# Optimization experiments

Hardware: AMD Instinct MI355X
Metric: run time of the kernel (lower is better)

## Reference

```python
import jax, jax.numpy as jnp
import numpy as np

NUM_CAPSULE = 32
DIM_CAPSULE = 16
ROUTINGS = 3
IN_CAPS = 144
IN_DIM = 8
EPS = 1e-7  # keras.backend.epsilon()


def setup_inputs() -> dict:
    key = jax.random.key(0)
    k1, k2 = jax.random.split(key)
    inputs = jax.random.normal(k1, (512, IN_CAPS, IN_DIM), dtype=jnp.float32)
    # glorot_uniform over shape [num_capsule, 144, dim_capsule, 8]
    fan_in, fan_out = IN_CAPS * IN_DIM, NUM_CAPSULE * DIM_CAPSULE
    limit = np.sqrt(6.0 / (fan_in + fan_out)).astype(np.float32)
    W = jax.random.uniform(k2, (NUM_CAPSULE, IN_CAPS, DIM_CAPSULE, IN_DIM),
                           minval=-limit, maxval=limit, dtype=jnp.float32)
    return {"inputs": inputs, "W": W}


def _squash(s):
    # s: [..., dim_capsule]
    n2 = jnp.sum(s * s, axis=-1, keepdims=True)
    return (n2 / (1.0 + n2)) * s / jnp.sqrt(n2 + EPS)


def reference(inputs, W):
    # inputs: [B, 144, 8]; W: [num_capsule, 144, dim_capsule, 8]
    # tile+einsum('abci,bcji->abcj') == broadcasted contraction over i
    inputs_hat = jnp.einsum('aci,bcji->abcj', inputs, W)  # [B, nc, 144, dc]
    b = jnp.zeros(inputs_hat.shape[:3], dtype=inputs_hat.dtype)  # [B, nc, 144]
    outputs = None
    for i in range(ROUTINGS):
        c = jax.nn.softmax(b, axis=1)                      # over num_capsule
        s = jnp.einsum('abc,abcd->abd', c, inputs_hat)     # [B, nc, dc]
        outputs = _squash(s)
        if i < ROUTINGS - 1:
            b = b + jnp.einsum('abd,abcd->abc', outputs, inputs_hat)
    return outputs
```

## Files before the change

### kernel.cpp

```cpp
#include <hip/hip_runtime.h>

#define NC 32
#define DC 16
#define INC 144
#define IND 8
#define NT 512

#define HBS 1168
#define HH_OFF (NC * HBS + 8)
#define LGW_OFF (HH_OFF + NC * HBS)
#define LG_S 152
#define OH_OFF (LGW_OFF + NC * LG_S)
#define SMEM_HALVES (OH_OFF + NC * DC)
#define SMEM_BYTES (SMEM_HALVES * 2)

typedef _Float16 h2 __attribute__((ext_vector_type(2)));
typedef _Float16 h4 __attribute__((ext_vector_type(4)));
typedef _Float16 h8 __attribute__((ext_vector_type(8)));
typedef float f4 __attribute__((ext_vector_type(4)));

union H8 { h8 v; h2 p[4]; };

#if __has_builtin(__builtin_amdgcn_fdot2)
__device__ __forceinline__ float fdot2(h2 a, h2 b, float c) {
    return __builtin_amdgcn_fdot2(a, b, c, false);
}
#else
__device__ __forceinline__ float fdot2(h2 a, h2 b, float c) {
    return c + (float)a[0] * (float)b[0] + (float)a[1] * (float)b[1];
}
#endif

__global__ void convw_kernel(const float* __restrict__ W, _Float16* __restrict__ Wh) {
    int i = blockIdx.x * 256 + threadIdx.x;
    f4 v = reinterpret_cast<const f4*>(W)[i];
    h4 h;
    h[0] = (_Float16)v[0]; h[1] = (_Float16)v[1];
    h[2] = (_Float16)v[2]; h[3] = (_Float16)v[3];
    reinterpret_cast<h4*>(Wh)[i] = h;
}

__device__ __forceinline__ float squash16(float s) {
    float n2 = s * s;
    n2 += __shfl_xor(n2, 1, 16);
    n2 += __shfl_xor(n2, 2, 16);
    n2 += __shfl_xor(n2, 4, 16);
    n2 += __shfl_xor(n2, 8, 16);
    return s * (n2 / ((1.0f + n2) * sqrtf(n2 + 1e-7f)));
}

template <typename WT>
__global__ __launch_bounds__(NT)
void caps_kernel(const float* __restrict__ xg, const WT* __restrict__ Wg,
                 float* __restrict__ out) {
    extern __shared__ _Float16 sm[];
    _Float16* lg = sm + LGW_OFF;
    _Float16* o_h = sm + OH_OFF;
    _Float16* x_h = lg;

    const int t = threadIdx.x;
    const int b = t >> 4;
    const int d = t & 15;
    const int a = blockIdx.x;

    if (t < (INC * IND) / 4) {
        f4 v = reinterpret_cast<const f4*>(xg + (size_t)a * (INC * IND))[t];
        h4 h;
        h[0] = (_Float16)v[0]; h[1] = (_Float16)v[1];
        h[2] = (_Float16)v[2]; h[3] = (_Float16)v[3];
        *reinterpret_cast<h4*>(x_h + t * 4) = h;
    }
    __syncthreads();

    _Float16* hw = sm + (d < 8 ? (b * HBS + d) : (HH_OFF + b * HBS + (d - 8)));

    float s0 = 0.0f;
    {
        const WT* wp = Wg + ((size_t)(b * INC) * DC + d) * IND;
        #pragma unroll 8
        for (int c = 0; c < INC; ++c) {
            H8 xv;
            xv.v = *reinterpret_cast<const h8*>(x_h + c * IND);
            float acc;
            if constexpr (sizeof(WT) == 2) {
                H8 wv;
                wv.v = *reinterpret_cast<const h8*>(wp + (size_t)c * (DC * IND));
                acc = fdot2(wv.p[0], xv.p[0], 0.f);
                acc = fdot2(wv.p[1], xv.p[1], acc);
                acc = fdot2(wv.p[2], xv.p[2], acc);
                acc = fdot2(wv.p[3], xv.p[3], acc);
            } else {
                const float* wf = reinterpret_cast<const float*>(wp) + (size_t)c * (DC * IND);
                f4 w0 = *reinterpret_cast<const f4*>(wf);
                f4 w1 = *reinterpret_cast<const f4*>(wf + 4);
                acc = (float)xv.v[0] * w0[0];
                acc = fmaf((float)xv.v[1], w0[1], acc);
                acc = fmaf((float)xv.v[2], w0[2], acc);
                acc = fmaf((float)xv.v[3], w0[3], acc);
                acc = fmaf((float)xv.v[4], w1[0], acc);
                acc = fmaf((float)xv.v[5], w1[1], acc);
                acc = fmaf((float)xv.v[6], w1[2], acc);
                acc = fmaf((float)xv.v[7], w1[3], acc);
            }
            s0 += acc;
            hw[c * 8] = (_Float16)acc;
            (void)0;
        }
    }
    {
        float o0 = squash16(s0 * (1.0f / 32.0f));
        o_h[t] = (_Float16)o0;
    }
    __syncthreads();

    float lgr[9] = {0.f, 0.f, 0.f, 0.f, 0.f, 0.f, 0.f, 0.f, 0.f};

    for (int it = 0; it < 2; ++it) {
        {
            H8 oL, oH;
            oL.v = *reinterpret_cast<const h8*>(o_h + b * DC);
            oH.v = *reinterpret_cast<const h8*>(o_h + b * DC + 8);
            #pragma unroll
            for (int k = 0; k < 9; ++k) {
                const int c = d + DC * k;
                H8 hl, hh;
                hl.v = *reinterpret_cast<const h8*>(sm + b * HBS + c * 8);
                hh.v = *reinterpret_cast<const h8*>(sm + HH_OFF + b * HBS + c * 8);
                float dot = fdot2(hl.p[0], oL.p[0], 0.f);
                dot = fdot2(hl.p[1], oL.p[1], dot);
                dot = fdot2(hl.p[2], oL.p[2], dot);
                dot = fdot2(hl.p[3], oL.p[3], dot);
                dot = fdot2(hh.p[0], oH.p[0], dot);
                dot = fdot2(hh.p[1], oH.p[1], dot);
                dot = fdot2(hh.p[2], oH.p[2], dot);
                dot = fdot2(hh.p[3], oH.p[3], dot);
                lgr[k] += dot;
                lg[b * LG_S + c] = (_Float16)lgr[k];
            }
        }
        __syncthreads();

        if (t < INC) {
            const int c = t;
            float m = -1e30f;
            for (int bb = 0; bb < NC; ++bb)
                m = fmaxf(m, (float)lg[bb * LG_S + c]);
            float S = 0.f;
            for (int bb = 0; bb < NC; ++bb) {
                float e = __expf((float)lg[bb * LG_S + c] - m);
                S += e;
                lg[bb * LG_S + c] = (_Float16)e;
            }
            float inv = 1.0f / S;
            for (int bb = 0; bb < NC; ++bb)
                lg[bb * LG_S + c] = (_Float16)((float)lg[bb * LG_S + c] * inv);
        }
        __syncthreads();

        {
            const _Float16* cp = lg + b * LG_S;
            float s = 0.f;
            #pragma unroll 8
            for (int c = 0; c < INC; ++c)
                s = fmaf((float)cp[c], (float)hw[c * 8], s);
            float oo = squash16(s);
            if (it == 0) {
                o_h[t] = (_Float16)oo;
            } else {
                out[(size_t)a * (NC * DC) + t] = oo;
            }
        }
        if (it == 0) __syncthreads();
    }
}

extern "C" void kernel_launch(void* const* d_in, const int* in_sizes, int n_in,
                              void* d_out, int out_size, void* d_ws, size_t ws_size,
                              hipStream_t stream) {
    const float* x = (const float*)d_in[0];
    const float* W = (const float*)d_in[1];
    float* out = (float*)d_out;

    const size_t WH_BYTES = (size_t)NC * INC * DC * IND * 2;

    if (ws_size >= WH_BYTES) {
        _Float16* Wh = (_Float16*)d_ws;
        hipLaunchKernelGGL(convw_kernel, dim3((NC * INC * DC * IND / 4) / 256),
                           dim3(256), 0, stream, W, Wh);
        hipFuncSetAttribute(reinterpret_cast<const void*>(&caps_kernel<_Float16>),
                            hipFuncAttributeMaxDynamicSharedMemorySize, SMEM_BYTES);
        hipLaunchKernelGGL(caps_kernel<_Float16>, dim3(512), dim3(NT), SMEM_BYTES,
                           stream, x, Wh, out);
    } else {
        hipFuncSetAttribute(reinterpret_cast<const void*>(&caps_kernel<float>),
                            hipFuncAttributeMaxDynamicSharedMemorySize, SMEM_BYTES);
        hipLaunchKernelGGL(caps_kernel<float>, dim3(512), dim3(NT), SMEM_BYTES,
                           stream, x, W, out);
    }
}
```

Measured before the change: 53.54 us.

## Split capsule routing across 1024 threads with transposed logits and parallel softmax

Doubles the block to 1024 threads, splitting the 144 input capsules into two halves whose partial sums are combined through shared memory. The logits are stored transposed (input-capsule-major) so the softmax reads contiguous rows, and two threads share each softmax with vector loads and a shuffle reduction. The intent is to cut the per-thread serial work and the slow strided softmax. The cost is extra barriers and partial-sum exchanges, and the larger block may cut occupancy or raise register pressure under the new launch bound.

```diff
diff --git a/kernel.cpp b/kernel.cpp
--- a/kernel.cpp
+++ b/kernel.cpp
@@ -4,14 +4,15 @@
 #define DC 16
 #define INC 144
 #define IND 8
-#define NT 512
+#define NT 1024
 
 #define HBS 1168
 #define HH_OFF (NC * HBS + 8)
-#define LGW_OFF (HH_OFF + NC * HBS)
-#define LG_S 152
-#define OH_OFF (LGW_OFF + NC * LG_S)
-#define SMEM_HALVES (OH_OFF + NC * DC)
+#define LGT_OFF (HH_OFF + NC * HBS)
+#define LGT_S 36
+#define OH_OFF (LGT_OFF + INC * LGT_S)
+#define PS_OFF (OH_OFF + NC * DC)
+#define SMEM_HALVES (PS_OFF + 512 * 2)
 #define SMEM_BYTES (SMEM_HALVES * 2)
 
 typedef _Float16 h2 __attribute__((ext_vector_type(2)));
@@ -50,25 +51,29 @@
 }
 
 template <typename WT>
-__global__ __launch_bounds__(NT)
+__global__ __launch_bounds__(NT, 4)
 void caps_kernel(const float* __restrict__ xg, const WT* __restrict__ Wg,
                  float* __restrict__ out) {
     extern __shared__ _Float16 sm[];
-    _Float16* lg = sm + LGW_OFF;
+    _Float16* lg = sm + LGT_OFF;
     _Float16* o_h = sm + OH_OFF;
+    float* ps = reinterpret_cast<float*>(sm + PS_OFF);
     _Float16* x_h = lg;
 
     const int t = threadIdx.x;
-    const int b = t >> 4;
-    const int d = t & 15;
+    const int h = t >> 9;
+    const int u = t & 511;
+    const int b = u >> 4;
+    const int d = u & 15;
     const int a = blockIdx.x;
+    const int c0 = h * 72;
 
     if (t < (INC * IND) / 4) {
         f4 v = reinterpret_cast<const f4*>(xg + (size_t)a * (INC * IND))[t];
-        h4 h;
-        h[0] = (_Float16)v[0]; h[1] = (_Float16)v[1];
-        h[2] = (_Float16)v[2]; h[3] = (_Float16)v[3];
-        *reinterpret_cast<h4*>(x_h + t * 4) = h;
+        h4 hv;
+        hv[0] = (_Float16)v[0]; hv[1] = (_Float16)v[1];
+        hv[2] = (_Float16)v[2]; hv[3] = (_Float16)v[3];
+        *reinterpret_cast<h4*>(x_h + t * 4) = hv;
     }
     __syncthreads();
 
@@ -76,21 +81,21 @@
 
     float s0 = 0.0f;
     {
-        const WT* wp = Wg + ((size_t)(b * INC) * DC + d) * IND;
+        const WT* wp = Wg + ((size_t)(b * INC + c0) * DC + d) * IND;
         #pragma unroll 8
-        for (int c = 0; c < INC; ++c) {
+        for (int c = c0; c < c0 + 72; ++c) {
             H8 xv;
             xv.v = *reinterpret_cast<const h8*>(x_h + c * IND);
             float acc;
             if constexpr (sizeof(WT) == 2) {
                 H8 wv;
-                wv.v = *reinterpret_cast<const h8*>(wp + (size_t)c * (DC * IND));
+                wv.v = *reinterpret_cast<const h8*>(wp);
                 acc = fdot2(wv.p[0], xv.p[0], 0.f);
                 acc = fdot2(wv.p[1], xv.p[1], acc);
                 acc = fdot2(wv.p[2], xv.p[2], acc);
                 acc = fdot2(wv.p[3], xv.p[3], acc);
             } else {
-                const float* wf = reinterpret_cast<const float*>(wp) + (size_t)c * (DC * IND);
+                const float* wf = reinterpret_cast<const float*>(wp);
                 f4 w0 = *reinterpret_cast<const f4*>(wf);
                 f4 w1 = *reinterpret_cast<const f4*>(wf + 4);
                 acc = (float)xv.v[0] * w0[0];
@@ -102,18 +107,21 @@
                 acc = fmaf((float)xv.v[6], w1[2], acc);
                 acc = fmaf((float)xv.v[7], w1[3], acc);
             }
+            wp += DC * IND;
             s0 += acc;
             hw[c * 8] = (_Float16)acc;
-            (void)0;
-        }
-    }
-    {
-        float o0 = squash16(s0 * (1.0f / 32.0f));
-        o_h[t] = (_Float16)o0;
-    }
+        }
+    }
+    if (h) ps[u] = s0;
     __syncthreads();
-
-    float lgr[9] = {0.f, 0.f, 0.f, 0.f, 0.f, 0.f, 0.f, 0.f, 0.f};
+    if (!h) {
+        float s0t = s0 + ps[u];
+        o_h[u] = (_Float16)squash16(s0t * (1.0f / 32.0f));
+    }
+    __syncthreads();
+
+    const int NK = h ? 4 : 5;
+    float lgr[5] = {0.f, 0.f, 0.f, 0.f, 0.f};
 
     for (int it = 0; it < 2; ++it) {
         {
@@ -121,56 +129,75 @@
             oL.v = *reinterpret_cast<const h8*>(o_h + b * DC);
             oH.v = *reinterpret_cast<const h8*>(o_h + b * DC + 8);
             #pragma unroll
-            for (int k = 0; k < 9; ++k) {
-                const int c = d + DC * k;
-                H8 hl, hh;
-                hl.v = *reinterpret_cast<const h8*>(sm + b * HBS + c * 8);
-                hh.v = *reinterpret_cast<const h8*>(sm + HH_OFF + b * HBS + c * 8);
-                float dot = fdot2(hl.p[0], oL.p[0], 0.f);
-                dot = fdot2(hl.p[1], oL.p[1], dot);
-                dot = fdot2(hl.p[2], oL.p[2], dot);
-                dot = fdot2(hl.p[3], oL.p[3], dot);
-                dot = fdot2(hh.p[0], oH.p[0], dot);
-                dot = fdot2(hh.p[1], oH.p[1], dot);
-                dot = fdot2(hh.p[2], oH.p[2], dot);
-                dot = fdot2(hh.p[3], oH.p[3], dot);
-                lgr[k] += dot;
-                lg[b * LG_S + c] = (_Float16)lgr[k];
+            for (int q = 0; q < 5; ++q) {
+                if (q < NK) {
+                    const int c = d + DC * (h + 2 * q);
+                    H8 hl, hu;
+                    hl.v = *reinterpret_cast<const h8*>(sm + b * HBS + c * 8);
+                    hu.v = *reinterpret_cast<const h8*>(sm + HH_OFF + b * HBS + c * 8);
+                    float dot = fdot2(hl.p[0], oL.p[0], 0.f);
+                    dot = fdot2(hl.p[1], oL.p[1], dot);
+                    dot = fdot2(hl.p[2], oL.p[2], dot);
+                    dot = fdot2(hl.p[3], oL.p[3], dot);
+                    dot = fdot2(hu.p[0], oH.p[0], dot);
+                    dot = fdot2(hu.p[1], oH.p[1], dot);
+                    dot = fdot2(hu.p[2], oH.p[2], dot);
+                    dot = fdot2(hu.p[3], oH.p[3], dot);
+                    lgr[q] += dot;
+                    lg[c * LGT_S + b] = (_Float16)lgr[q];
+                }
             }
         }
         __syncthreads();
 
-        if (t < INC) {
-            const int c = t;
-            float m = -1e30f;
-            for (int bb = 0; bb < NC; ++bb)
-                m = fmaxf(m, (float)lg[bb * LG_S + c]);
+        if (t < 2 * INC) {
+            const int c = t >> 1;
+            const int hh = t & 1;
+            _Float16* row = lg + c * LGT_S + hh * 16;
+            float v[16];
+            #pragma unroll
+            for (int j = 0; j < 4; ++j) {
+                h4 r = *reinterpret_cast<const h4*>(row + 4 * j);
+                v[4 * j + 0] = (float)r[0]; v[4 * j + 1] = (float)r[1];
+                v[4 * j + 2] = (float)r[2]; v[4 * j + 3] = (float)r[3];
+            }
+            float m = v[0];
+            #pragma unroll
+            for (int j = 1; j < 16; ++j) m = fmaxf(m, v[j]);
+            m = fmaxf(m, __shfl_xor(m, 1));
             float S = 0.f;
-            for (int bb = 0; bb < NC; ++bb) {
-                float e = __expf((float)lg[bb * LG_S + c] - m);
-                S += e;
-                lg[bb * LG_S + c] = (_Float16)e;
-            }
+            #pragma unroll
+            for (int j = 0; j < 16; ++j) { v[j] = __expf(v[j] - m); S += v[j]; }
+            S += __shfl_xor(S, 1);
             float inv = 1.0f / S;
-            for (int bb = 0; bb < NC; ++bb)
-                lg[bb * LG_S + c] = (_Float16)((float)lg[bb * LG_S + c] * inv);
+            #pragma unroll
+            for (int j = 0; j < 4; ++j) {
+                h4 r;
+                r[0] = (_Float16)(v[4 * j + 0] * inv);
+                r[1] = (_Float16)(v[4 * j + 1] * inv);
+                r[2] = (_Float16)(v[4 * j + 2] * inv);
+                r[3] = (_Float16)(v[4 * j + 3] * inv);
+                *reinterpret_cast<h4*>(row + 4 * j) = r;
+            }
         }
         __syncthreads();
 
         {
-            const _Float16* cp = lg + b * LG_S;
+            const _Float16* cp0 = lg + b;
             float s = 0.f;
             #pragma unroll 8
-            for (int c = 0; c < INC; ++c)
-                s = fmaf((float)cp[c], (float)hw[c * 8], s);
-            float oo = squash16(s);
-            if (it == 0) {
-                o_h[t] = (_Float16)oo;
-            } else {
-                out[(size_t)a * (NC * DC) + t] = oo;
-            }
-        }
-        if (it == 0) __syncthreads();
+            for (int c = c0; c < c0 + 72; ++c)
+                s = fmaf((float)cp0[c * LGT_S], (float)hw[c * 8], s);
+            if (h) ps[u] = s;
+            __syncthreads();
+            if (!h) {
+                float st = s + ps[u];
+                float oo = squash16(st);
+                if (it == 0) o_h[u] = (_Float16)oo;
+                else out[(size_t)a * (NC * DC) + u] = oo;
+            }
+            if (it == 0) __syncthreads();
+        }
     }
 }
 
```

Result: no change. 52.82 us (-1.3%).

## Keep inputs_hat in registers and compute agreement via packed-half shuffle reductions

Applied to the files above, without the earlier changes.

Each thread now holds its 144 fp16 inputs_hat values in registers (72 packed halves) instead of writing them to a large shared-memory buffer. The agreement dot products use a butterfly reduce-scatter with shuffles inside each 16-lane group, and the softmax is split across two threads per input capsule using register arrays. Shared memory drops to a small static allocation, which removes the dynamic-smem attribute call and may let more blocks fit per CU. The cost is heavy register pressure from 72 h2 registers plus full unrolling, which could cap occupancy or cause spills, and more of the reduction now runs in fp16.

```diff
diff --git a/kernel.cpp b/kernel.cpp
--- a/kernel.cpp
+++ b/kernel.cpp
@@ -1,18 +1,12 @@
 #include <hip/hip_runtime.h>
+#include <utility>
 
 #define NC 32
 #define DC 16
 #define INC 144
 #define IND 8
 #define NT 512
-
-#define HBS 1168
-#define HH_OFF (NC * HBS + 8)
-#define LGW_OFF (HH_OFF + NC * HBS)
 #define LG_S 152
-#define OH_OFF (LGW_OFF + NC * LG_S)
-#define SMEM_HALVES (OH_OFF + NC * DC)
-#define SMEM_BYTES (SMEM_HALVES * 2)
 
 typedef _Float16 h2 __attribute__((ext_vector_type(2)));
 typedef _Float16 h4 __attribute__((ext_vector_type(4)));
@@ -20,6 +14,16 @@
 typedef float f4 __attribute__((ext_vector_type(4)));
 
 union H8 { h8 v; h2 p[4]; };
+union HU { h2 h; unsigned u; };
+
+template <class F, int... Is>
+__device__ __forceinline__ void sfor_impl(F&& f, std::integer_sequence<int, Is...>) {
+    (f(std::integral_constant<int, Is>{}), ...);
+}
+template <int N, class F>
+__device__ __forceinline__ void sfor(F&& f) {
+    sfor_impl((F&&)f, std::make_integer_sequence<int, N>{});
+}
 
 #if __has_builtin(__builtin_amdgcn_fdot2)
 __device__ __forceinline__ float fdot2(h2 a, h2 b, float c) {
@@ -53,10 +57,8 @@
 __global__ __launch_bounds__(NT)
 void caps_kernel(const float* __restrict__ xg, const WT* __restrict__ Wg,
                  float* __restrict__ out) {
-    extern __shared__ _Float16 sm[];
-    _Float16* lg = sm + LGW_OFF;
-    _Float16* o_h = sm + OH_OFF;
-    _Float16* x_h = lg;
+    __shared__ _Float16 x_h[INC * IND];
+    __shared__ _Float16 lg[NC * LG_S];
 
     const int t = threadIdx.x;
     const int b = t >> 4;
@@ -65,20 +67,19 @@
 
     if (t < (INC * IND) / 4) {
         f4 v = reinterpret_cast<const f4*>(xg + (size_t)a * (INC * IND))[t];
-        h4 h;
-        h[0] = (_Float16)v[0]; h[1] = (_Float16)v[1];
-        h[2] = (_Float16)v[2]; h[3] = (_Float16)v[3];
-        *reinterpret_cast<h4*>(x_h + t * 4) = h;
+        h4 hv;
+        hv[0] = (_Float16)v[0]; hv[1] = (_Float16)v[1];
+        hv[2] = (_Float16)v[2]; hv[3] = (_Float16)v[3];
+        *reinterpret_cast<h4*>(x_h + t * 4) = hv;
     }
     __syncthreads();
 
-    _Float16* hw = sm + (d < 8 ? (b * HBS + d) : (HH_OFF + b * HBS + (d - 8)));
-
+    h2 hreg[72];
     float s0 = 0.0f;
     {
         const WT* wp = Wg + ((size_t)(b * INC) * DC + d) * IND;
-        #pragma unroll 8
-        for (int c = 0; c < INC; ++c) {
+        sfor<INC>([&](auto C) {
+            constexpr int c = C.value;
             H8 xv;
             xv.v = *reinterpret_cast<const h8*>(x_h + c * IND);
             float acc;
@@ -103,74 +104,113 @@
                 acc = fmaf((float)xv.v[7], w1[3], acc);
             }
             s0 += acc;
-            hw[c * 8] = (_Float16)acc;
-            (void)0;
-        }
-    }
-    {
-        float o0 = squash16(s0 * (1.0f / 32.0f));
-        o_h[t] = (_Float16)o0;
-    }
-    __syncthreads();
-
-    float lgr[9] = {0.f, 0.f, 0.f, 0.f, 0.f, 0.f, 0.f, 0.f, 0.f};
+            hreg[c >> 1][c & 1] = (_Float16)acc;
+        });
+    }
+    float o = squash16(s0 * (1.0f / 32.0f));
+
+    float lgr[9];
+    sfor<9>([&](auto J) { lgr[J.value] = 0.f; });
 
     for (int it = 0; it < 2; ++it) {
         {
-            H8 oL, oH;
-            oL.v = *reinterpret_cast<const h8*>(o_h + b * DC);
-            oH.v = *reinterpret_cast<const h8*>(o_h + b * DC + 8);
-            #pragma unroll
-            for (int k = 0; k < 9; ++k) {
-                const int c = d + DC * k;
-                H8 hl, hh;
-                hl.v = *reinterpret_cast<const h8*>(sm + b * HBS + c * 8);
-                hh.v = *reinterpret_cast<const h8*>(sm + HH_OFF + b * HBS + c * 8);
-                float dot = fdot2(hl.p[0], oL.p[0], 0.f);
-                dot = fdot2(hl.p[1], oL.p[1], dot);
-                dot = fdot2(hl.p[2], oL.p[2], dot);
-                dot = fdot2(hl.p[3], oL.p[3], dot);
-                dot = fdot2(hh.p[0], oH.p[0], dot);
-                dot = fdot2(hh.p[1], oH.p[1], dot);
-                dot = fdot2(hh.p[2], oH.p[2], dot);
-                dot = fdot2(hh.p[3], oH.p[3], dot);
-                lgr[k] += dot;
-                lg[b * LG_S + c] = (_Float16)lgr[k];
-            }
+            h2 oh2;
+            oh2[0] = (_Float16)o; oh2[1] = (_Float16)o;
+            sfor<9>([&](auto J) {
+                constexpr int j = J.value;
+                h2 qp[8];
+                sfor<8>([&](auto I) {
+                    constexpr int i = I.value;
+                    qp[i] = oh2 * hreg[8 * j + i];
+                });
+                const bool h8s = (d & 8) != 0;
+                sfor<4>([&](auto I) {
+                    constexpr int i = I.value;
+                    h2 send = h8s ? qp[i] : qp[i + 4];
+                    h2 keep = h8s ? qp[i + 4] : qp[i];
+                    HU su; su.h = send;
+                    HU ru; ru.u = __shfl_xor(su.u, 8, 16);
+                    qp[i] = keep + ru.h;
+                });
+                const bool h4s = (d & 4) != 0;
+                sfor<2>([&](auto I) {
+                    constexpr int i = I.value;
+                    h2 send = h4s ? qp[i] : qp[i + 2];
+                    h2 keep = h4s ? qp[i + 2] : qp[i];
+                    HU su; su.h = send;
+                    HU ru; ru.u = __shfl_xor(su.u, 4, 16);
+                    qp[i] = keep + ru.h;
+                });
+                {
+                    const bool h2s = (d & 2) != 0;
+                    h2 send = h2s ? qp[0] : qp[1];
+                    h2 keep = h2s ? qp[1] : qp[0];
+                    HU su; su.h = send;
+                    HU ru; ru.u = __shfl_xor(su.u, 2, 16);
+                    qp[0] = keep + ru.h;
+                }
+                {
+                    HU su; su.h = qp[0];
+                    HU ru; ru.u = __shfl_xor(su.u, 1, 16);
+                    h2 tot = qp[0] + ru.h;
+                    HU tu; tu.h = tot;
+                    unsigned short sel = (d & 1) ? (unsigned short)(tu.u >> 16)
+                                                 : (unsigned short)(tu.u & 0xffffu);
+                    union { unsigned short s; _Float16 hv; } cv;
+                    cv.s = sel;
+                    lgr[j] += (float)cv.hv;
+                }
+                lg[b * LG_S + 16 * j + d] = (_Float16)lgr[j];
+            });
         }
         __syncthreads();
 
-        if (t < INC) {
-            const int c = t;
-            float m = -1e30f;
-            for (int bb = 0; bb < NC; ++bb)
-                m = fmaxf(m, (float)lg[bb * LG_S + c]);
+        if (t < 2 * INC) {
+            const int c = t >> 1;
+            const int hh = t & 1;
+            float v[16];
+            sfor<16>([&](auto I) {
+                constexpr int i = I.value;
+                v[i] = (float)lg[(hh * 16 + i) * LG_S + c];
+            });
+            float m = v[0];
+            sfor<15>([&](auto I) { m = fmaxf(m, v[I.value + 1]); });
+            m = fmaxf(m, __shfl_xor(m, 1));
             float S = 0.f;
-            for (int bb = 0; bb < NC; ++bb) {
-                float e = __expf((float)lg[bb * LG_S + c] - m);
-                S += e;
-                lg[bb * LG_S + c] = (_Float16)e;
-            }
+            sfor<16>([&](auto I) {
+                constexpr int i = I.value;
+                v[i] = __expf(v[i] - m);
+                S += v[i];
+            });
+            S += __shfl_xor(S, 1);
             float inv = 1.0f / S;
-            for (int bb = 0; bb < NC; ++bb)
-                lg[bb * LG_S + c] = (_Float16)((float)lg[bb * LG_S + c] * inv);
+            sfor<16>([&](auto I) {
+                constexpr int i = I.value;
+                lg[(hh * 16 + i) * LG_S + c] = (_Float16)(v[i] * inv);
+            });
         }
         __syncthreads();
 
         {
             const _Float16* cp = lg + b * LG_S;
-            float s = 0.f;
-            #pragma unroll 8
-            for (int c = 0; c < INC; ++c)
-                s = fmaf((float)cp[c], (float)hw[c * 8], s);
-            float oo = squash16(s);
+            float sA = 0.f, sB = 0.f;
+            sfor<18>([&](auto M) {
+                constexpr int m2 = M.value;
+                H8 cc;
+                cc.v = *reinterpret_cast<const h8*>(cp + m2 * 8);
+                sA = fdot2(cc.p[0], hreg[m2 * 4 + 0], sA);
+                sB = fdot2(cc.p[1], hreg[m2 * 4 + 1], sB);
+                sA = fdot2(cc.p[2], hreg[m2 * 4 + 2], sA);
+                sB = fdot2(cc.p[3], hreg[m2 * 4 + 3], sB);
+            });
+            float oo = squash16(sA + sB);
             if (it == 0) {
-                o_h[t] = (_Float16)oo;
+                o = oo;
+                __syncthreads();
             } else {
                 out[(size_t)a * (NC * DC) + t] = oo;
             }
         }
-        if (it == 0) __syncthreads();
     }
 }
 
@@ -187,14 +227,10 @@
         _Float16* Wh = (_Float16*)d_ws;
         hipLaunchKernelGGL(convw_kernel, dim3((NC * INC * DC * IND / 4) / 256),
                            dim3(256), 0, stream, W, Wh);
-        hipFuncSetAttribute(reinterpret_cast<const void*>(&caps_kernel<_Float16>),
-                            hipFuncAttributeMaxDynamicSharedMemorySize, SMEM_BYTES);
-        hipLaunchKernelGGL(caps_kernel<_Float16>, dim3(512), dim3(NT), SMEM_BYTES,
+        hipLaunchKernelGGL(caps_kernel<_Float16>, dim3(512), dim3(NT), 0,
                            stream, x, Wh, out);
     } else {
-        hipFuncSetAttribute(reinterpret_cast<const void*>(&caps_kernel<float>),
-                            hipFuncAttributeMaxDynamicSharedMemorySize, SMEM_BYTES);
-        hipLaunchKernelGGL(caps_kernel<float>, dim3(512), dim3(NT), SMEM_BYTES,
+        hipLaunchKernelGGL(caps_kernel<float>, dim3(512), dim3(NT), 0,
                            stream, x, W, out);
     }
 }
```

Result: slower. 70.01 us (+30.8%).

## Keep inputs_hat in registers and reorder W for coalesced per-thread capsule loads

Applied to the files above, without the earlier changes.

Each thread now owns 9 input capsules for one output capsule and holds all 16 inputs_hat dimensions in registers, instead of spilling the full inputs_hat tensor into ~150KB of shared memory. The W conversion kernel reorders W into a layout that matches this thread mapping so fp16 loads coalesce. Softmax is split across two threads per input capsule with shuffles, and the squash reduction runs through cross-lane butterflies. This removes the large LDS footprint to allow more blocks per CU, at the cost of heavy register use (18 h8 vectors plus 16 accumulators) and many shuffles.

```diff
diff --git a/kernel.cpp b/kernel.cpp
--- a/kernel.cpp
+++ b/kernel.cpp
@@ -5,21 +5,14 @@
 #define INC 144
 #define IND 8
 #define NT 512
-
-#define HBS 1168
-#define HH_OFF (NC * HBS + 8)
-#define LGW_OFF (HH_OFF + NC * HBS)
 #define LG_S 152
-#define OH_OFF (LGW_OFF + NC * LG_S)
-#define SMEM_HALVES (OH_OFF + NC * DC)
-#define SMEM_BYTES (SMEM_HALVES * 2)
 
 typedef _Float16 h2 __attribute__((ext_vector_type(2)));
-typedef _Float16 h4 __attribute__((ext_vector_type(4)));
+typedef _Float16 h4v __attribute__((ext_vector_type(4)));
 typedef _Float16 h8 __attribute__((ext_vector_type(8)));
 typedef float f4 __attribute__((ext_vector_type(4)));
 
-union H8 { h8 v; h2 p[4]; };
+union H8 { h8 v; h2 p[4]; _Float16 e[8]; };
 
 #if __has_builtin(__builtin_amdgcn_fdot2)
 __device__ __forceinline__ float fdot2(h2 a, h2 b, float c) {
@@ -33,144 +26,187 @@
 
 __global__ void convw_kernel(const float* __restrict__ W, _Float16* __restrict__ Wh) {
     int i = blockIdx.x * 256 + threadIdx.x;
-    f4 v = reinterpret_cast<const f4*>(W)[i];
-    h4 h;
-    h[0] = (_Float16)v[0]; h[1] = (_Float16)v[1];
-    h[2] = (_Float16)v[2]; h[3] = (_Float16)v[3];
-    reinterpret_cast<h4*>(Wh)[i] = h;
-}
-
-__device__ __forceinline__ float squash16(float s) {
-    float n2 = s * s;
-    n2 += __shfl_xor(n2, 1, 16);
-    n2 += __shfl_xor(n2, 2, 16);
-    n2 += __shfl_xor(n2, 4, 16);
-    n2 += __shfl_xor(n2, 8, 16);
-    return s * (n2 / ((1.0f + n2) * sqrtf(n2 + 1e-7f)));
-}
+    int cg = i & 15, d = (i >> 4) & 15, bk = i >> 8;
+    int k = bk % 9, b = bk / 9;
+    const float* s = W + (((size_t)b * INC + cg + 16 * k) * DC + d) * IND;
+    f4 v0 = *reinterpret_cast<const f4*>(s);
+    f4 v1 = *reinterpret_cast<const f4*>(s + 4);
+    H8 o;
+    o.e[0] = (_Float16)v0[0]; o.e[1] = (_Float16)v0[1];
+    o.e[2] = (_Float16)v0[2]; o.e[3] = (_Float16)v0[3];
+    o.e[4] = (_Float16)v1[0]; o.e[5] = (_Float16)v1[1];
+    o.e[6] = (_Float16)v1[2]; o.e[7] = (_Float16)v1[3];
+    *reinterpret_cast<h8*>(Wh + (size_t)i * 8) = o.v;
+}
+
+#define R9(M)  M(0) M(1) M(2) M(3) M(4) M(5) M(6) M(7) M(8)
+#define R16(M) M(0) M(1) M(2) M(3) M(4) M(5) M(6) M(7) M(8) M(9) M(10) M(11) M(12) M(13) M(14) M(15)
 
 template <typename WT>
 __global__ __launch_bounds__(NT)
+__attribute__((amdgpu_waves_per_eu(2, 4)))
 void caps_kernel(const float* __restrict__ xg, const WT* __restrict__ Wg,
                  float* __restrict__ out) {
-    extern __shared__ _Float16 sm[];
-    _Float16* lg = sm + LGW_OFF;
-    _Float16* o_h = sm + OH_OFF;
-    _Float16* x_h = lg;
+    __shared__ __align__(16) _Float16 x_h[INC * IND];
+    __shared__ __align__(16) _Float16 lg[NC * LG_S];
 
     const int t = threadIdx.x;
     const int b = t >> 4;
-    const int d = t & 15;
+    const int cg = t & 15;
     const int a = blockIdx.x;
 
-    if (t < (INC * IND) / 4) {
+    if (t < 288) {
         f4 v = reinterpret_cast<const f4*>(xg + (size_t)a * (INC * IND))[t];
-        h4 h;
-        h[0] = (_Float16)v[0]; h[1] = (_Float16)v[1];
-        h[2] = (_Float16)v[2]; h[3] = (_Float16)v[3];
-        *reinterpret_cast<h4*>(x_h + t * 4) = h;
+        h4v hv;
+        hv[0] = (_Float16)v[0]; hv[1] = (_Float16)v[1];
+        hv[2] = (_Float16)v[2]; hv[3] = (_Float16)v[3];
+        *reinterpret_cast<h4v*>(x_h + t * 4) = hv;
     }
     __syncthreads();
 
-    _Float16* hw = sm + (d < 8 ? (b * HBS + d) : (HH_OFF + b * HBS + (d - 8)));
-
-    float s0 = 0.0f;
-    {
-        const WT* wp = Wg + ((size_t)(b * INC) * DC + d) * IND;
-        #pragma unroll 8
-        for (int c = 0; c < INC; ++c) {
-            H8 xv;
-            xv.v = *reinterpret_cast<const h8*>(x_h + c * IND);
-            float acc;
-            if constexpr (sizeof(WT) == 2) {
-                H8 wv;
-                wv.v = *reinterpret_cast<const h8*>(wp + (size_t)c * (DC * IND));
-                acc = fdot2(wv.p[0], xv.p[0], 0.f);
-                acc = fdot2(wv.p[1], xv.p[1], acc);
-                acc = fdot2(wv.p[2], xv.p[2], acc);
-                acc = fdot2(wv.p[3], xv.p[3], acc);
-            } else {
-                const float* wf = reinterpret_cast<const float*>(wp) + (size_t)c * (DC * IND);
-                f4 w0 = *reinterpret_cast<const f4*>(wf);
-                f4 w1 = *reinterpret_cast<const f4*>(wf + 4);
-                acc = (float)xv.v[0] * w0[0];
-                acc = fmaf((float)xv.v[1], w0[1], acc);
-                acc = fmaf((float)xv.v[2], w0[2], acc);
-                acc = fmaf((float)xv.v[3], w0[3], acc);
-                acc = fmaf((float)xv.v[4], w1[0], acc);
-                acc = fmaf((float)xv.v[5], w1[1], acc);
-                acc = fmaf((float)xv.v[6], w1[2], acc);
-                acc = fmaf((float)xv.v[7], w1[3], acc);
-            }
-            s0 += acc;
-            hw[c * 8] = (_Float16)acc;
-            (void)0;
-        }
-    }
-    {
-        float o0 = squash16(s0 * (1.0f / 32.0f));
-        o_h[t] = (_Float16)o0;
-    }
-    __syncthreads();
-
-    float lgr[9] = {0.f, 0.f, 0.f, 0.f, 0.f, 0.f, 0.f, 0.f, 0.f};
+#define DECLH(K) h8 hc##K##L, hc##K##H;
+    R9(DECLH)
+#define DECLS(D) float s##D;
+    R16(DECLS)
+#define ZEROS(D) s##D = 0.f;
+
+#define HD1(T, E, DG) { \
+    float ac; \
+    if constexpr (sizeof(WT) == 2) { \
+        H8 w; w.v = *reinterpret_cast<const h8*>(wr + (DG) * 128 + cg * 8); \
+        ac = fdot2(w.p[0], xv.p[0], 0.f); \
+        ac = fdot2(w.p[1], xv.p[1], ac); \
+        ac = fdot2(w.p[2], xv.p[2], ac); \
+        ac = fdot2(w.p[3], xv.p[3], ac); \
+    } else { \
+        const float* wf = reinterpret_cast<const float*>(wr) + (DG) * IND; \
+        f4 w0 = *reinterpret_cast<const f4*>(wf); \
+        f4 w1 = *reinterpret_cast<const f4*>(wf + 4); \
+        ac = (float)xv.e[0] * w0[0]; \
+        ac = fmaf((float)xv.e[1], w0[1], ac); \
+        ac = fmaf((float)xv.e[2], w0[2], ac); \
+        ac = fmaf((float)xv.e[3], w0[3], ac); \
+        ac = fmaf((float)xv.e[4], w1[0], ac); \
+        ac = fmaf((float)xv.e[5], w1[1], ac); \
+        ac = fmaf((float)xv.e[6], w1[2], ac); \
+        ac = fmaf((float)xv.e[7], w1[3], ac); \
+    } \
+    T.e[E] = (_Float16)ac; s##DG += ac; }
+
+#define HSTEP(K) { \
+    const int c = cg + 16 * (K); \
+    H8 xv; xv.v = *reinterpret_cast<const h8*>(x_h + c * IND); \
+    const WT* wr; \
+    if constexpr (sizeof(WT) == 2) wr = Wg + ((size_t)(b * 9 + (K)) * 2048); \
+    else wr = Wg + ((size_t)(b * INC + c) * (DC * IND)); \
+    H8 tL, tH; \
+    HD1(tL,0,0) HD1(tL,1,1) HD1(tL,2,2) HD1(tL,3,3) \
+    HD1(tL,4,4) HD1(tL,5,5) HD1(tL,6,6) HD1(tL,7,7) \
+    HD1(tH,0,8) HD1(tH,1,9) HD1(tH,2,10) HD1(tH,3,11) \
+    HD1(tH,4,12) HD1(tH,5,13) HD1(tH,6,14) HD1(tH,7,15) \
+    hc##K##L = tL.v; hc##K##H = tH.v; }
+
+    R16(ZEROS)
+    R9(HSTEP)
+
+#define BF1(D) s##D += __shfl_xor(s##D, 1, 16);
+#define BF2(D) s##D += __shfl_xor(s##D, 2, 16);
+#define BF4(D) s##D += __shfl_xor(s##D, 4, 16);
+#define BF8(D) s##D += __shfl_xor(s##D, 8, 16);
+#define SCL(D) s##D *= (1.0f / 32.0f);
+    R16(BF1) R16(BF2) R16(BF4) R16(BF8)
+    R16(SCL)
+
+#define SUMSQ (s0*s0+s1*s1+s2*s2+s3*s3+s4*s4+s5*s5+s6*s6+s7*s7+ \
+               s8*s8+s9*s9+s10*s10+s11*s11+s12*s12+s13*s13+s14*s14+s15*s15)
+
+    h8 oLv, oHv;
+#define PACKO { \
+    float n2 = SUMSQ; \
+    float ff = n2 / ((1.0f + n2) * sqrtf(n2 + 1e-7f)); \
+    H8 pl, ph; \
+    pl.e[0]=(_Float16)(s0*ff);  pl.e[1]=(_Float16)(s1*ff); \
+    pl.e[2]=(_Float16)(s2*ff);  pl.e[3]=(_Float16)(s3*ff); \
+    pl.e[4]=(_Float16)(s4*ff);  pl.e[5]=(_Float16)(s5*ff); \
+    pl.e[6]=(_Float16)(s6*ff);  pl.e[7]=(_Float16)(s7*ff); \
+    ph.e[0]=(_Float16)(s8*ff);  ph.e[1]=(_Float16)(s9*ff); \
+    ph.e[2]=(_Float16)(s10*ff); ph.e[3]=(_Float16)(s11*ff); \
+    ph.e[4]=(_Float16)(s12*ff); ph.e[5]=(_Float16)(s13*ff); \
+    ph.e[6]=(_Float16)(s14*ff); ph.e[7]=(_Float16)(s15*ff); \
+    oLv = pl.v; oHv = ph.v; }
+    PACKO
+
+#define DECLG(K) float lgr##K = 0.f;
+    R9(DECLG)
+
+#define BSTEP(K) { \
+    H8 hl, hh; hl.v = hc##K##L; hh.v = hc##K##H; \
+    H8 ol, oh; ol.v = oLv; oh.v = oHv; \
+    float dt = fdot2(hl.p[0], ol.p[0], 0.f); \
+    dt = fdot2(hl.p[1], ol.p[1], dt); \
+    dt = fdot2(hl.p[2], ol.p[2], dt); \
+    dt = fdot2(hl.p[3], ol.p[3], dt); \
+    dt = fdot2(hh.p[0], oh.p[0], dt); \
+    dt = fdot2(hh.p[1], oh.p[1], dt); \
+    dt = fdot2(hh.p[2], oh.p[2], dt); \
+    dt = fdot2(hh.p[3], oh.p[3], dt); \
+    lgr##K += dt; \
+    lg[b * LG_S + cg + 16 * (K)] = (_Float16)lgr##K; }
+
+#define SSTEP(K) { \
+    float cf = (float)lg[b * LG_S + cg + 16 * (K)]; \
+    H8 hl, hh; hl.v = hc##K##L; hh.v = hc##K##H; \
+    s0  = fmaf(cf, (float)hl.e[0], s0);  s1  = fmaf(cf, (float)hl.e[1], s1); \
+    s2  = fmaf(cf, (float)hl.e[2], s2);  s3  = fmaf(cf, (float)hl.e[3], s3); \
+    s4  = fmaf(cf, (float)hl.e[4], s4);  s5  = fmaf(cf, (float)hl.e[5], s5); \
+    s6  = fmaf(cf, (float)hl.e[6], s6);  s7  = fmaf(cf, (float)hl.e[7], s7); \
+    s8  = fmaf(cf, (float)hh.e[0], s8);  s9  = fmaf(cf, (float)hh.e[1], s9); \
+    s10 = fmaf(cf, (float)hh.e[2], s10); s11 = fmaf(cf, (float)hh.e[3], s11); \
+    s12 = fmaf(cf, (float)hh.e[4], s12); s13 = fmaf(cf, (float)hh.e[5], s13); \
+    s14 = fmaf(cf, (float)hh.e[6], s14); s15 = fmaf(cf, (float)hh.e[7], s15); }
 
     for (int it = 0; it < 2; ++it) {
-        {
-            H8 oL, oH;
-            oL.v = *reinterpret_cast<const h8*>(o_h + b * DC);
-            oH.v = *reinterpret_cast<const h8*>(o_h + b * DC + 8);
-            #pragma unroll
-            for (int k = 0; k < 9; ++k) {
-                const int c = d + DC * k;
-                H8 hl, hh;
-                hl.v = *reinterpret_cast<const h8*>(sm + b * HBS + c * 8);
-                hh.v = *reinterpret_cast<const h8*>(sm + HH_OFF + b * HBS + c * 8);
-                float dot = fdot2(hl.p[0], oL.p[0], 0.f);
-                dot = fdot2(hl.p[1], oL.p[1], dot);
-                dot = fdot2(hl.p[2], oL.p[2], dot);
-                dot = fdot2(hl.p[3], oL.p[3], dot);
-                dot = fdot2(hh.p[0], oH.p[0], dot);
-                dot = fdot2(hh.p[1], oH.p[1], dot);
-                dot = fdot2(hh.p[2], oH.p[2], dot);
-                dot = fdot2(hh.p[3], oH.p[3], dot);
-                lgr[k] += dot;
-                lg[b * LG_S + c] = (_Float16)lgr[k];
-            }
+        R9(BSTEP)
+        __syncthreads();
+
+        if (t < 2 * INC) {
+            const int c = t >> 1;
+            const int rb = (t & 1) * 16;
+#define SMR(I) float v##I = (float)lg[(rb + I) * LG_S + c];
+            R16(SMR)
+            float m = fmaxf(v0, v1);
+#define SMM(I) m = fmaxf(m, v##I);
+            SMM(2) SMM(3) SMM(4) SMM(5) SMM(6) SMM(7) SMM(8) SMM(9)
+            SMM(10) SMM(11) SMM(12) SMM(13) SMM(14) SMM(15)
+            m = fmaxf(m, __shfl_xor(m, 1));
+            float S = 0.f;
+#define SME(I) v##I = __expf(v##I - m); S += v##I;
+            R16(SME)
+            S += __shfl_xor(S, 1);
+            float inv = 1.0f / S;
+#define SMW(I) lg[(rb + I) * LG_S + c] = (_Float16)(v##I * inv);
+            R16(SMW)
         }
         __syncthreads();
 
-        if (t < INC) {
-            const int c = t;
-            float m = -1e30f;
-            for (int bb = 0; bb < NC; ++bb)
-                m = fmaxf(m, (float)lg[bb * LG_S + c]);
-            float S = 0.f;
-            for (int bb = 0; bb < NC; ++bb) {
-                float e = __expf((float)lg[bb * LG_S + c] - m);
-                S += e;
-                lg[bb * LG_S + c] = (_Float16)e;
-            }
-            float inv = 1.0f / S;
-            for (int bb = 0; bb < NC; ++bb)
-                lg[bb * LG_S + c] = (_Float16)((float)lg[bb * LG_S + c] * inv);
+        R16(ZEROS)
+        R9(SSTEP)
+        R16(BF1) R16(BF2) R16(BF4) R16(BF8)
+
+        if (it == 0) {
+            PACKO
+            __syncthreads();
+        } else {
+            float n2 = SUMSQ;
+            float ff = n2 / ((1.0f + n2) * sqrtf(n2 + 1e-7f));
+            float r = s0;
+            if (cg == 1) r = s1;   if (cg == 2) r = s2;   if (cg == 3) r = s3;
+            if (cg == 4) r = s4;   if (cg == 5) r = s5;   if (cg == 6) r = s6;
+            if (cg == 7) r = s7;   if (cg == 8) r = s8;   if (cg == 9) r = s9;
+            if (cg == 10) r = s10; if (cg == 11) r = s11; if (cg == 12) r = s12;
+            if (cg == 13) r = s13; if (cg == 14) r = s14; if (cg == 15) r = s15;
+            out[(size_t)a * (NC * DC) + t] = r * ff;
         }
-        __syncthreads();
-
-        {
-            const _Float16* cp = lg + b * LG_S;
-            float s = 0.f;
-            #pragma unroll 8
-            for (int c = 0; c < INC; ++c)
-                s = fmaf((float)cp[c], (float)hw[c * 8], s);
-            float oo = squash16(s);
-            if (it == 0) {
-                o_h[t] = (_Float16)oo;
-            } else {
-                out[(size_t)a * (NC * DC) + t] = oo;
-            }
-        }
-        if (it == 0) __syncthreads();
     }
 }
 
@@ -185,16 +221,11 @@
 
     if (ws_size >= WH_BYTES) {
         _Float16* Wh = (_Float16*)d_ws;
-        hipLaunchKernelGGL(convw_kernel, dim3((NC * INC * DC * IND / 4) / 256),
-                           dim3(256), 0, stream, W, Wh);
-        hipFuncSetAttribute(reinterpret_cast<const void*>(&caps_kernel<_Float16>),
-                            hipFuncAttributeMaxDynamicSharedMemorySize, SMEM_BYTES);
-        hipLaunchKernelGGL(caps_kernel<_Float16>, dim3(512), dim3(NT), SMEM_BYTES,
+        hipLaunchKernelGGL(convw_kernel, dim3(288), dim3(256), 0, stream, W, Wh);
+        hipLaunchKernelGGL(caps_kernel<_Float16>, dim3(512), dim3(NT), 0,
                            stream, x, Wh, out);
     } else {
-        hipFuncSetAttribute(reinterpret_cast<const void*>(&caps_kernel<float>),
-                            hipFuncAttributeMaxDynamicSharedMemorySize, SMEM_BYTES);
-        hipLaunchKernelGGL(caps_kernel<float>, dim3(512), dim3(NT), SMEM_BYTES,
+        hipLaunchKernelGGL(caps_kernel<float>, dim3(512), dim3(NT), 0,
                            stream, x, W, out);
     }
 }
```

New measurement: 56.40 us. 1.05x slower.
